# Optimization experiments

Measured on AMD Instinct MI355X. Metric: run time of the kernel, lower is better.

## Reference

```python
import jax, jax.numpy as jnp
import numpy as np

N_HEADS = 12
D_MODEL = 768
D_HEAD = 64
N_CTX = 2048
ROTARY_DIM = 64
ROTARY_BASE = 10000.0
IGNORE = -100000.0


def _sin_cos_rotary(rotary_dim, n_ctx, base):
    # rotary_adjacent_pairs = False -> freq tiled as (2 d)
    pos = jnp.arange(n_ctx, dtype=jnp.float32)
    dim = jnp.arange(rotary_dim // 2, dtype=jnp.float32)
    freq = base ** (dim / (rotary_dim / 2))
    freq = jnp.concatenate([freq, freq])  # '(2 d)'
    angles = pos[:, None] / freq[None, :]  # [n_ctx, rotary_dim]
    return jnp.sin(angles), jnp.cos(angles)


def _apply_rotary(x, sin, cos):
    # x: [B, S, H, d_head]
    S = x.shape[1]
    x_rot = x[..., :ROTARY_DIM]
    x_pass = x[..., ROTARY_DIM:]
    n = ROTARY_DIM // 2
    # rotate: first half <- -second half, second half <- first half
    x_flip = jnp.concatenate([-x_rot[..., n:], x_rot[..., :n]], axis=-1)
    c = cos[None, :S, None, :]
    s = sin[None, :S, None, :]
    return jnp.concatenate([x_rot * c + x_flip * s, x_pass], axis=-1)


def setup_inputs() -> dict:
    key = jax.random.key(0)
    ks = jax.random.split(key, 10)
    B, S = 2, 2048
    x_shape = (B, S, N_HEADS, D_MODEL)
    inp = {
        "normalized_resid_pre_q": jax.random.normal(ks[0], x_shape, jnp.float32),
        "normalized_resid_pre_k": jax.random.normal(ks[1], x_shape, jnp.float32),
        "normalized_resid_pre_v": jax.random.normal(ks[2], x_shape, jnp.float32),
        "W_Q": jax.random.normal(ks[3], (N_HEADS, D_MODEL, D_HEAD), jnp.float32) * 0.02,
        "b_Q": jnp.zeros((N_HEADS, D_HEAD), jnp.float32),
        "W_K": jax.random.normal(ks[4], (N_HEADS, D_MODEL, D_HEAD), jnp.float32) * 0.02,
        "b_K": jnp.zeros((N_HEADS, D_HEAD), jnp.float32),
        "W_V": jax.random.normal(ks[5], (N_HEADS, D_MODEL, D_HEAD), jnp.float32) * 0.02,
        "b_V": jnp.zeros((N_HEADS, D_HEAD), jnp.float32),
        "W_O": jax.random.normal(ks[6], (N_HEADS, D_HEAD, D_MODEL), jnp.float32) * 0.02,
        "b_O": jnp.zeros((D_MODEL,), jnp.float32),
    }
    return inp


def reference(normalized_resid_pre_q, normalized_resid_pre_k, normalized_resid_pre_v,
              W_Q, b_Q, W_K, b_K, W_V, b_V, W_O, b_O):
    sin, cos = _sin_cos_rotary(ROTARY_DIM, N_CTX, ROTARY_BASE)
    # per-head QKV projections: [B,S,H,M] x [H,M,D] -> [B,S,H,D]
    q = jnp.einsum('bshm,hmd->bshd', normalized_resid_pre_q, W_Q) + b_Q
    k = jnp.einsum('bshm,hmd->bshd', normalized_resid_pre_k, W_K) + b_K
    q = _apply_rotary(q, sin, cos)
    k = _apply_rotary(k, sin, cos)
    scores = jnp.einsum('bqhd,bkhd->bhqk', q, k) / jnp.sqrt(jnp.float32(D_HEAD))
    S = scores.shape[-1]
    causal = jnp.triu(jnp.ones((S, S), dtype=bool), k=1)
    scores = jnp.where(causal, jnp.float32(IGNORE), scores)
    pattern = jax.nn.softmax(scores, axis=-1)
    v = jnp.einsum('bkhm,hmd->bkhd', normalized_resid_pre_v, W_V) + b_V
    z = jnp.einsum('bhqk,bkhd->bqhd', pattern, v)
    # output keeps the head axis: [B,S,H,d_model]; b_O is divided by n_heads
    attn_out = jnp.einsum('bqhd,hdm->bqhm', z, W_O) + b_O / N_HEADS
    return attn_out
```

## Files before the change

kernel.cpp:

```cpp
#include <hip/hip_runtime.h>
#include <hip/hip_bf16.h>

typedef __bf16 bf16x8 __attribute__((ext_vector_type(8)));
typedef float f32x4 __attribute__((ext_vector_type(4)));
typedef unsigned short ushort8 __attribute__((ext_vector_type(8)));

static_assert(sizeof(bf16x8) == 16, "bf16x8 must be 16B");

#define NH 12
#define SEQ 2048
#define DM 768
#define DH 64
#define NB 2

static __device__ __forceinline__ unsigned short f2bf(float f) {
    __hip_bfloat16 h = __float2bfloat16(f);
    return __builtin_bit_cast(unsigned short, h);
}
static __device__ __forceinline__ bf16x8 ld_bf8(const unsigned short* p) {
    ushort8 u = *(const ushort8*)p;
    return __builtin_bit_cast(bf16x8, u);
}

__global__ __launch_bounds__(256) void kprep(
    const float* __restrict__ WQ, const float* __restrict__ WK,
    const float* __restrict__ WV, const float* __restrict__ WO,
    unsigned short* __restrict__ Wt, unsigned short* __restrict__ Wot)
{
    __shared__ __align__(16) unsigned short T[64 * 72];
    int bid = blockIdx.x;
    int tensor = bid / 144;
    int rem = bid % 144;
    int h = rem / 12, tile = rem % 12;
    const float* src; unsigned short* dst; int R, C, r0, c0;
    if (tensor < 3) {
        src = (tensor == 0 ? WQ : tensor == 1 ? WK : WV) + (size_t)h * DM * DH;
        dst = Wt + ((size_t)tensor * NH + h) * DH * DM;
        R = DM; C = DH; r0 = tile * 64; c0 = 0;
    } else {
        src = WO + (size_t)h * DH * DM;
        dst = Wot + (size_t)h * DM * DH;
        R = DH; C = DM; r0 = 0; c0 = tile * 64;
    }
    int t = threadIdx.x;
    int rr = t >> 2, cc0 = (t & 3) * 16;
    const float* sp = src + (size_t)(r0 + rr) * C + c0 + cc0;
#pragma unroll
    for (int i = 0; i < 4; i++) {
        float4 v = *(const float4*)(sp + 4 * i);
        T[(cc0 + 4 * i + 0) * 72 + rr] = f2bf(v.x);
        T[(cc0 + 4 * i + 1) * 72 + rr] = f2bf(v.y);
        T[(cc0 + 4 * i + 2) * 72 + rr] = f2bf(v.z);
        T[(cc0 + 4 * i + 3) * 72 + rr] = f2bf(v.w);
    }
    __syncthreads();
    int cc = t >> 2, ch = t & 3;
    ushort8 o0 = *(const ushort8*)&T[cc * 72 + ch * 16];
    ushort8 o1 = *(const ushort8*)&T[cc * 72 + ch * 16 + 8];
    unsigned short* dp = dst + (size_t)(c0 + cc) * R + r0 + ch * 16;
    *(ushort8*)dp = o0;
    *(ushort8*)(dp + 8) = o1;
}

__global__ __launch_bounds__(256) void kproj(
    const float* __restrict__ Xq, const float* __restrict__ Xk,
    const float* __restrict__ Xv, const unsigned short* __restrict__ Wt,
    const float* __restrict__ bQ, const float* __restrict__ bK,
    const float* __restrict__ bV,
    unsigned short* __restrict__ Qw, unsigned short* __restrict__ Kw,
    unsigned short* __restrict__ Vtw)
{
    __shared__ __align__(16) unsigned short sm[64 * 72];
    int bid = blockIdx.x;
    int p  = bid / 768;
    int b  = (bid / 384) & 1;
    int h  = (bid / 32) % 12;
    int st = bid & 31;
    const float* X = p == 0 ? Xq : (p == 1 ? Xk : Xv);
    int t = threadIdx.x;
    int w = t >> 6, lane = t & 63, l = lane & 15, quad = lane >> 4;

    const float* xrow = X + (((size_t)(b * SEQ + st * 64 + 16 * w + l)) * NH + h) * DM + quad * 8;
    const unsigned short* wbase = Wt + ((size_t)(p * NH + h)) * DH * DM;

    f32x4 acc[4] = {};
    for (int k0 = 0; k0 < DM; k0 += 32) {
        float4 f0 = *(const float4*)(xrow + k0);
        float4 f1 = *(const float4*)(xrow + k0 + 4);
        ushort8 u;
        u[0] = f2bf(f0.x); u[1] = f2bf(f0.y); u[2] = f2bf(f0.z); u[3] = f2bf(f0.w);
        u[4] = f2bf(f1.x); u[5] = f2bf(f1.y); u[6] = f2bf(f1.z); u[7] = f2bf(f1.w);
        bf16x8 a = __builtin_bit_cast(bf16x8, u);
#pragma unroll
        for (int nt = 0; nt < 4; nt++) {
            bf16x8 bf = ld_bf8(wbase + ((size_t)(16 * nt + l)) * DM + k0 + quad * 8);
            acc[nt] = __builtin_amdgcn_mfma_f32_16x16x32_bf16(a, bf, acc[nt], 0, 0, 0);
        }
    }

    const float* bias = p == 0 ? bQ : (p == 1 ? bK : bV);
#pragma unroll
    for (int nt = 0; nt < 4; nt++) {
        float bv = bias[h * DH + 16 * nt + l];
#pragma unroll
        for (int r = 0; r < 4; r++) acc[nt][r] += bv;
    }

    if (p < 2) {
        const float L2B = 13.287712379549449f;
        float inv1 = exp2f(-((float)l)        * (L2B / 32.0f));
        float inv2 = exp2f(-((float)(l + 16)) * (L2B / 32.0f));
#pragma unroll
        for (int r = 0; r < 4; r++) {
            float pos = (float)(st * 64 + 16 * w + quad * 4 + r);
            float s1, c1, s2, c2;
            sincosf(pos * inv1, &s1, &c1);
            sincosf(pos * inv2, &s2, &c2);
            float a0 = acc[0][r], a1 = acc[1][r], a2 = acc[2][r], a3 = acc[3][r];
            acc[0][r] = a0 * c1 - a2 * s1;
            acc[1][r] = a1 * c2 - a3 * s2;
            acc[2][r] = a2 * c1 + a0 * s1;
            acc[3][r] = a3 * c2 + a1 * s2;
        }
        unsigned short* dst = (p == 0 ? Qw : Kw) + (((size_t)(b * NH + h)) * SEQ + st * 64) * DH;
#pragma unroll
        for (int nt = 0; nt < 4; nt++)
#pragma unroll
            for (int r = 0; r < 4; r++)
                dst[(16 * w + quad * 4 + r) * DH + 16 * nt + l] = f2bf(acc[nt][r]);
    } else {
#pragma unroll
        for (int nt = 0; nt < 4; nt++)
#pragma unroll
            for (int r = 0; r < 4; r++)
                sm[(16 * nt + l) * 72 + 16 * w + quad * 4 + r] = f2bf(acc[nt][r]);
        __syncthreads();
        int d = t >> 2, c = t & 3;
        ushort8 v0 = *(const ushort8*)&sm[d * 72 + c * 16];
        ushort8 v1 = *(const ushort8*)&sm[d * 72 + c * 16 + 8];
        unsigned short* dp = Vtw + (((size_t)(b * NH + h)) * DH + d) * SEQ + st * 64 + c * 16;
        *(ushort8*)dp = v0;
        *(ushort8*)(dp + 8) = v1;
    }
}

__global__ __launch_bounds__(256) void kattn(
    const unsigned short* __restrict__ Qw, const unsigned short* __restrict__ Kw,
    const unsigned short* __restrict__ Vtw, unsigned short* __restrict__ Zw)
{
    __shared__ __align__(16) unsigned short sK[64 * 72];
    __shared__ __align__(16) unsigned short sV[64 * 72];
    __shared__ __align__(16) unsigned short sP[64 * 72];
    int bid = blockIdx.x;
    int b = bid / 384;
    int h = (bid / 32) % 12;
    int qt = 31 - (bid & 31);
    int t = threadIdx.x;
    int w = t >> 6, lane = t & 63, l = lane & 15, quad = lane >> 4;
    int q0 = qt * 64;

    const unsigned short* qbase = Qw + (((size_t)(b * NH + h)) * SEQ + q0 + 16 * w + l) * DH;
    bf16x8 qf0 = ld_bf8(qbase + quad * 8);
    bf16x8 qf1 = ld_bf8(qbase + 32 + quad * 8);

    const unsigned short* kb = Kw + ((size_t)(b * NH + h)) * SEQ * DH;
    const unsigned short* vb = Vtw + ((size_t)(b * NH + h)) * DH * SEQ;

    int srow = t >> 2, sc = (t & 3) * 16;

    float m_i[4], l_i[4];
    f32x4 zacc[4] = {};
#pragma unroll
    for (int r = 0; r < 4; r++) { m_i[r] = -1e30f; l_i[r] = 0.0f; }

    for (int kt = 0; kt <= qt; kt++) {
        __syncthreads();
        {
            const unsigned short* ks = kb + (size_t)(kt * 64 + srow) * DH + sc;
            ushort8 a0 = *(const ushort8*)ks;
            ushort8 a1 = *(const ushort8*)(ks + 8);
            *(ushort8*)&sK[srow * 72 + sc] = a0;
            *(ushort8*)&sK[srow * 72 + sc + 8] = a1;
            const unsigned short* vs = vb + (size_t)srow * SEQ + kt * 64 + sc;
            ushort8 b0 = *(const ushort8*)vs;
            ushort8 b1 = *(const ushort8*)(vs + 8);
            *(ushort8*)&sV[srow * 72 + sc] = b0;
            *(ushort8*)&sV[srow * 72 + sc + 8] = b1;
        }
        __syncthreads();

        f32x4 sacc[4] = {};
#pragma unroll
        for (int nt = 0; nt < 4; nt++) {
            bf16x8 k0f = __builtin_bit_cast(bf16x8, *(const ushort8*)&sK[(16 * nt + l) * 72 + quad * 8]);
            sacc[nt] = __builtin_amdgcn_mfma_f32_16x16x32_bf16(qf0, k0f, sacc[nt], 0, 0, 0);
            bf16x8 k1f = __builtin_bit_cast(bf16x8, *(const ushort8*)&sK[(16 * nt + l) * 72 + 32 + quad * 8]);
            sacc[nt] = __builtin_amdgcn_mfma_f32_16x16x32_bf16(qf1, k1f, sacc[nt], 0, 0, 0);
        }
        bool diag = (kt == qt);
#pragma unroll
        for (int nt = 0; nt < 4; nt++)
#pragma unroll
            for (int r = 0; r < 4; r++) {
                float s = sacc[nt][r] * 0.125f;
                if (diag && (16 * nt + l) > (16 * w + quad * 4 + r)) s = -1e30f;
                sacc[nt][r] = s;
            }
        float newm[4], alpha[4];
#pragma unroll
        for (int r = 0; r < 4; r++) {
            float rm = fmaxf(fmaxf(sacc[0][r], sacc[1][r]), fmaxf(sacc[2][r], sacc[3][r]));
            rm = fmaxf(rm, __shfl_xor(rm, 1));
            rm = fmaxf(rm, __shfl_xor(rm, 2));
            rm = fmaxf(rm, __shfl_xor(rm, 4));
            rm = fmaxf(rm, __shfl_xor(rm, 8));
            float nm = fmaxf(m_i[r], rm);
            alpha[r] = __expf(m_i[r] - nm);
            m_i[r] = nm;
            newm[r] = nm;
        }
#pragma unroll
        for (int r = 0; r < 4; r++) {
            float rs = 0.0f;
#pragma unroll
            for (int nt = 0; nt < 4; nt++) {
                float pv = __expf(sacc[nt][r] - newm[r]);
                sacc[nt][r] = pv;
                rs += pv;
            }
            rs += __shfl_xor(rs, 1);
            rs += __shfl_xor(rs, 2);
            rs += __shfl_xor(rs, 4);
            rs += __shfl_xor(rs, 8);
            l_i[r] = l_i[r] * alpha[r] + rs;
            zacc[0][r] *= alpha[r]; zacc[1][r] *= alpha[r];
            zacc[2][r] *= alpha[r]; zacc[3][r] *= alpha[r];
        }
#pragma unroll
        for (int nt = 0; nt < 4; nt++)
#pragma unroll
            for (int r = 0; r < 4; r++)
                sP[(w * 16 + quad * 4 + r) * 72 + 16 * nt + l] = f2bf(sacc[nt][r]);
        __asm__ volatile("s_waitcnt lgkmcnt(0)" ::: "memory");
        bf16x8 pa0 = __builtin_bit_cast(bf16x8, *(const ushort8*)&sP[(w * 16 + l) * 72 + quad * 8]);
        bf16x8 pa1 = __builtin_bit_cast(bf16x8, *(const ushort8*)&sP[(w * 16 + l) * 72 + 32 + quad * 8]);
#pragma unroll
        for (int nt = 0; nt < 4; nt++) {
            bf16x8 v0f = __builtin_bit_cast(bf16x8, *(const ushort8*)&sV[(16 * nt + l) * 72 + quad * 8]);
            zacc[nt] = __builtin_amdgcn_mfma_f32_16x16x32_bf16(pa0, v0f, zacc[nt], 0, 0, 0);
            bf16x8 v1f = __builtin_bit_cast(bf16x8, *(const ushort8*)&sV[(16 * nt + l) * 72 + 32 + quad * 8]);
            zacc[nt] = __builtin_amdgcn_mfma_f32_16x16x32_bf16(pa1, v1f, zacc[nt], 0, 0, 0);
        }
    }
    unsigned short* zb = Zw + (((size_t)(b * NH + h)) * SEQ + q0) * DH;
#pragma unroll
    for (int r = 0; r < 4; r++) {
        float inv = 1.0f / l_i[r];
#pragma unroll
        for (int nt = 0; nt < 4; nt++)
            zb[(16 * w + quad * 4 + r) * DH + 16 * nt + l] = f2bf(zacc[nt][r] * inv);
    }
}

__global__ __launch_bounds__(256) void kout(
    const unsigned short* __restrict__ Zw, const unsigned short* __restrict__ Wot,
    const float* __restrict__ bO, float* __restrict__ out)
{
    int bid = blockIdx.x;
    int b = bid / 384;
    int h = (bid / 32) % 12;
    int st = bid & 31;
    int t = threadIdx.x;
    int w = t >> 6, lane = t & 63, l = lane & 15, quad = lane >> 4;

    const unsigned short* zbase = Zw + (((size_t)(b * NH + h)) * SEQ + st * 64 + 16 * w + l) * DH;
    bf16x8 za0 = ld_bf8(zbase + quad * 8);
    bf16x8 za1 = ld_bf8(zbase + 32 + quad * 8);
    const unsigned short* wbase = Wot + (size_t)h * DM * DH;
    float* obase = out + ((size_t)(b * SEQ + st * 64) * NH + h) * DM;

    for (int chunk = 0; chunk < 6; chunk++) {
        f32x4 acc[8] = {};
#pragma unroll
        for (int nt = 0; nt < 8; nt++) {
            int m = chunk * 128 + 16 * nt + l;
            bf16x8 w0 = ld_bf8(wbase + (size_t)m * DH + quad * 8);
            acc[nt] = __builtin_amdgcn_mfma_f32_16x16x32_bf16(za0, w0, acc[nt], 0, 0, 0);
            bf16x8 w1 = ld_bf8(wbase + (size_t)m * DH + 32 + quad * 8);
            acc[nt] = __builtin_amdgcn_mfma_f32_16x16x32_bf16(za1, w1, acc[nt], 0, 0, 0);
        }
#pragma unroll
        for (int nt = 0; nt < 8; nt++) {
            int m = chunk * 128 + 16 * nt + l;
            float bo = bO[m] * (1.0f / 12.0f);
#pragma unroll
            for (int r = 0; r < 4; r++) {
                int srow = 16 * w + quad * 4 + r;
                obase[(size_t)srow * NH * DM + m] = acc[nt][r] + bo;
            }
        }
    }
}

extern "C" void kernel_launch(void* const* d_in, const int* in_sizes, int n_in,
                              void* d_out, int out_size, void* d_ws, size_t ws_size,
                              hipStream_t stream) {
    const float* Xq = (const float*)d_in[0];
    const float* Xk = (const float*)d_in[1];
    const float* Xv = (const float*)d_in[2];
    const float* WQ = (const float*)d_in[3];
    const float* bQ = (const float*)d_in[4];
    const float* WK = (const float*)d_in[5];
    const float* bK = (const float*)d_in[6];
    const float* WV = (const float*)d_in[7];
    const float* bV = (const float*)d_in[8];
    const float* WO = (const float*)d_in[9];
    const float* bO = (const float*)d_in[10];
    float* out = (float*)d_out;

    char* ws = (char*)d_ws;
    size_t o = 0;
    const size_t qkv_bytes = (size_t)NB * NH * SEQ * DH * 2;
    unsigned short* Qw  = (unsigned short*)(ws + o); o += qkv_bytes;
    unsigned short* Kw  = (unsigned short*)(ws + o); o += qkv_bytes;
    unsigned short* Vtw = (unsigned short*)(ws + o); o += qkv_bytes;
    unsigned short* Zw  = (unsigned short*)(ws + o); o += qkv_bytes;
    unsigned short* Wt  = (unsigned short*)(ws + o); o += (size_t)3 * NH * DH * DM * 2;
    unsigned short* Wot = (unsigned short*)(ws + o); o += (size_t)NH * DM * DH * 2;

    kprep<<<dim3(576), dim3(256), 0, stream>>>(WQ, WK, WV, WO, Wt, Wot);
    kproj<<<dim3(2304), dim3(256), 0, stream>>>(Xq, Xk, Xv, Wt, bQ, bK, bV, Qw, Kw, Vtw);
    kattn<<<dim3(768), dim3(256), 0, stream>>>(Qw, Kw, Vtw, Zw);
    kout<<<dim3(768), dim3(256), 0, stream>>>(Zw, Wot, bO, out);
}
```

Baseline: 651.3 us.

## Batch projection loads, stage Q/K stores via LDS, prefetch K/V tiles, split output kernel

The projection kernel now loads four K-steps of X at once and gathers the weight fragments before each group of MFMAs, which gives more memory-level parallelism. Q/K results are staged through LDS so they can be written to global memory as 16-byte vectors instead of scattered 2-byte stores. The attention kernel prefetches the next K/V tile into registers while the current tile is being computed. The output kernel is split six ways across the model dimension to get more blocks, at the cost of reloading the Z fragments in each block.

New measurement: 627.5 us. -3.7%, faster.

```diff
diff --git a/kernel.cpp b/kernel.cpp
--- a/kernel.cpp
+++ b/kernel.cpp
@@ -19,6 +19,12 @@
 }
 static __device__ __forceinline__ bf16x8 ld_bf8(const unsigned short* p) {
     ushort8 u = *(const ushort8*)p;
+    return __builtin_bit_cast(bf16x8, u);
+}
+static __device__ __forceinline__ bf16x8 pack8(float4 f0, float4 f1) {
+    ushort8 u;
+    u[0] = f2bf(f0.x); u[1] = f2bf(f0.y); u[2] = f2bf(f0.z); u[3] = f2bf(f0.w);
+    u[4] = f2bf(f1.x); u[5] = f2bf(f1.y); u[6] = f2bf(f1.z); u[7] = f2bf(f1.w);
     return __builtin_bit_cast(bf16x8, u);
 }
 
@@ -81,20 +87,26 @@
     int w = t >> 6, lane = t & 63, l = lane & 15, quad = lane >> 4;
 
     const float* xrow = X + (((size_t)(b * SEQ + st * 64 + 16 * w + l)) * NH + h) * DM + quad * 8;
-    const unsigned short* wbase = Wt + ((size_t)(p * NH + h)) * DH * DM;
+    const unsigned short* wbase = Wt + ((size_t)(p * NH + h)) * DH * DM + (size_t)l * DM + quad * 8;
 
     f32x4 acc[4] = {};
-    for (int k0 = 0; k0 < DM; k0 += 32) {
-        float4 f0 = *(const float4*)(xrow + k0);
-        float4 f1 = *(const float4*)(xrow + k0 + 4);
-        ushort8 u;
-        u[0] = f2bf(f0.x); u[1] = f2bf(f0.y); u[2] = f2bf(f0.z); u[3] = f2bf(f0.w);
-        u[4] = f2bf(f1.x); u[5] = f2bf(f1.y); u[6] = f2bf(f1.z); u[7] = f2bf(f1.w);
-        bf16x8 a = __builtin_bit_cast(bf16x8, u);
-#pragma unroll
-        for (int nt = 0; nt < 4; nt++) {
-            bf16x8 bf = ld_bf8(wbase + ((size_t)(16 * nt + l)) * DM + k0 + quad * 8);
-            acc[nt] = __builtin_amdgcn_mfma_f32_16x16x32_bf16(a, bf, acc[nt], 0, 0, 0);
+    for (int k0 = 0; k0 < DM; k0 += 128) {
+        float4 xa[8];
+#pragma unroll
+        for (int u = 0; u < 4; u++) {
+            xa[2 * u]     = *(const float4*)(xrow + k0 + 32 * u);
+            xa[2 * u + 1] = *(const float4*)(xrow + k0 + 32 * u + 4);
+        }
+#pragma unroll
+        for (int u = 0; u < 4; u++) {
+            bf16x8 wf[4];
+#pragma unroll
+            for (int nt = 0; nt < 4; nt++)
+                wf[nt] = ld_bf8(wbase + (size_t)nt * 16 * DM + k0 + 32 * u);
+            bf16x8 a = pack8(xa[2 * u], xa[2 * u + 1]);
+#pragma unroll
+            for (int nt = 0; nt < 4; nt++)
+                acc[nt] = __builtin_amdgcn_mfma_f32_16x16x32_bf16(a, wf[nt], acc[nt], 0, 0, 0);
         }
     }
 
@@ -122,12 +134,19 @@
             acc[2][r] = a2 * c1 + a0 * s1;
             acc[3][r] = a3 * c2 + a1 * s2;
         }
-        unsigned short* dst = (p == 0 ? Qw : Kw) + (((size_t)(b * NH + h)) * SEQ + st * 64) * DH;
 #pragma unroll
         for (int nt = 0; nt < 4; nt++)
 #pragma unroll
             for (int r = 0; r < 4; r++)
-                dst[(16 * w + quad * 4 + r) * DH + 16 * nt + l] = f2bf(acc[nt][r]);
+                sm[(16 * w + quad * 4 + r) * 72 + 16 * nt + l] = f2bf(acc[nt][r]);
+        __asm__ volatile("s_waitcnt lgkmcnt(0)" ::: "memory");
+        int local = t & 63;
+        int row = 16 * w + (local >> 2), c = local & 3;
+        ushort8 q0 = *(const ushort8*)&sm[row * 72 + c * 16];
+        ushort8 q1 = *(const ushort8*)&sm[row * 72 + c * 16 + 8];
+        unsigned short* dst = (p == 0 ? Qw : Kw) + (((size_t)(b * NH + h)) * SEQ + st * 64 + row) * DH + c * 16;
+        *(ushort8*)dst = q0;
+        *(ushort8*)(dst + 8) = q1;
     } else {
 #pragma unroll
         for (int nt = 0; nt < 4; nt++)
@@ -173,21 +192,30 @@
 #pragma unroll
     for (int r = 0; r < 4; r++) { m_i[r] = -1e30f; l_i[r] = 0.0f; }
 
+    ushort8 pk0, pk1, pv0, pv1;
+    {
+        const unsigned short* ks = kb + (size_t)srow * DH + sc;
+        pk0 = *(const ushort8*)ks;
+        pk1 = *(const ushort8*)(ks + 8);
+        const unsigned short* vs = vb + (size_t)srow * SEQ + sc;
+        pv0 = *(const ushort8*)vs;
+        pv1 = *(const ushort8*)(vs + 8);
+    }
+
     for (int kt = 0; kt <= qt; kt++) {
+        *(ushort8*)&sK[srow * 72 + sc] = pk0;
+        *(ushort8*)&sK[srow * 72 + sc + 8] = pk1;
+        *(ushort8*)&sV[srow * 72 + sc] = pv0;
+        *(ushort8*)&sV[srow * 72 + sc + 8] = pv1;
         __syncthreads();
-        {
-            const unsigned short* ks = kb + (size_t)(kt * 64 + srow) * DH + sc;
-            ushort8 a0 = *(const ushort8*)ks;
-            ushort8 a1 = *(const ushort8*)(ks + 8);
-            *(ushort8*)&sK[srow * 72 + sc] = a0;
-            *(ushort8*)&sK[srow * 72 + sc + 8] = a1;
-            const unsigned short* vs = vb + (size_t)srow * SEQ + kt * 64 + sc;
-            ushort8 b0 = *(const ushort8*)vs;
-            ushort8 b1 = *(const ushort8*)(vs + 8);
-            *(ushort8*)&sV[srow * 72 + sc] = b0;
-            *(ushort8*)&sV[srow * 72 + sc + 8] = b1;
-        }
-        __syncthreads();
+        if (kt < qt) {
+            const unsigned short* ks = kb + (size_t)((kt + 1) * 64 + srow) * DH + sc;
+            pk0 = *(const ushort8*)ks;
+            pk1 = *(const ushort8*)(ks + 8);
+            const unsigned short* vs = vb + (size_t)srow * SEQ + (kt + 1) * 64 + sc;
+            pv0 = *(const ushort8*)vs;
+            pv1 = *(const ushort8*)(vs + 8);
+        }
 
         f32x4 sacc[4] = {};
 #pragma unroll
@@ -251,6 +279,7 @@
             bf16x8 v1f = __builtin_bit_cast(bf16x8, *(const ushort8*)&sV[(16 * nt + l) * 72 + 32 + quad * 8]);
             zacc[nt] = __builtin_amdgcn_mfma_f32_16x16x32_bf16(pa1, v1f, zacc[nt], 0, 0, 0);
         }
+        __syncthreads();
     }
     unsigned short* zb = Zw + (((size_t)(b * NH + h)) * SEQ + q0) * DH;
 #pragma unroll
@@ -267,37 +296,36 @@
     const float* __restrict__ bO, float* __restrict__ out)
 {
     int bid = blockIdx.x;
-    int b = bid / 384;
-    int h = (bid / 32) % 12;
-    int st = bid & 31;
+    int chunk = bid % 6;
+    int bh = bid / 6;
+    int b = bh / 384;
+    int h = (bh / 32) % 12;
+    int st = bh & 31;
     int t = threadIdx.x;
     int w = t >> 6, lane = t & 63, l = lane & 15, quad = lane >> 4;
 
     const unsigned short* zbase = Zw + (((size_t)(b * NH + h)) * SEQ + st * 64 + 16 * w + l) * DH;
     bf16x8 za0 = ld_bf8(zbase + quad * 8);
     bf16x8 za1 = ld_bf8(zbase + 32 + quad * 8);
-    const unsigned short* wbase = Wot + (size_t)h * DM * DH;
-    float* obase = out + ((size_t)(b * SEQ + st * 64) * NH + h) * DM;
-
-    for (int chunk = 0; chunk < 6; chunk++) {
-        f32x4 acc[8] = {};
-#pragma unroll
-        for (int nt = 0; nt < 8; nt++) {
-            int m = chunk * 128 + 16 * nt + l;
-            bf16x8 w0 = ld_bf8(wbase + (size_t)m * DH + quad * 8);
-            acc[nt] = __builtin_amdgcn_mfma_f32_16x16x32_bf16(za0, w0, acc[nt], 0, 0, 0);
-            bf16x8 w1 = ld_bf8(wbase + (size_t)m * DH + 32 + quad * 8);
-            acc[nt] = __builtin_amdgcn_mfma_f32_16x16x32_bf16(za1, w1, acc[nt], 0, 0, 0);
-        }
-#pragma unroll
-        for (int nt = 0; nt < 8; nt++) {
-            int m = chunk * 128 + 16 * nt + l;
-            float bo = bO[m] * (1.0f / 12.0f);
-#pragma unroll
-            for (int r = 0; r < 4; r++) {
-                int srow = 16 * w + quad * 4 + r;
-                obase[(size_t)srow * NH * DM + m] = acc[nt][r] + bo;
-            }
+    const unsigned short* wbase = Wot + (size_t)h * DM * DH + (size_t)(chunk * 128 + l) * DH + quad * 8;
+    float* obase = out + ((size_t)(b * SEQ + st * 64) * NH + h) * DM + chunk * 128;
+
+    f32x4 acc[8] = {};
+#pragma unroll
+    for (int nt = 0; nt < 8; nt++) {
+        bf16x8 w0 = ld_bf8(wbase + (size_t)nt * 16 * DH);
+        acc[nt] = __builtin_amdgcn_mfma_f32_16x16x32_bf16(za0, w0, acc[nt], 0, 0, 0);
+        bf16x8 w1 = ld_bf8(wbase + (size_t)nt * 16 * DH + 32);
+        acc[nt] = __builtin_amdgcn_mfma_f32_16x16x32_bf16(za1, w1, acc[nt], 0, 0, 0);
+    }
+#pragma unroll
+    for (int nt = 0; nt < 8; nt++) {
+        int m = 16 * nt + l;
+        float bo = bO[chunk * 128 + m] * (1.0f / 12.0f);
+#pragma unroll
+        for (int r = 0; r < 4; r++) {
+            int srow = 16 * w + quad * 4 + r;
+            obase[(size_t)srow * NH * DM + m] = acc[nt][r] + bo;
         }
     }
 }
@@ -331,5 +359,5 @@
     kprep<<<dim3(576), dim3(256), 0, stream>>>(WQ, WK, WV, WO, Wt, Wot);
     kproj<<<dim3(2304), dim3(256), 0, stream>>>(Xq, Xk, Xv, Wt, bQ, bK, bV, Qw, Kw, Vtw);
     kattn<<<dim3(768), dim3(256), 0, stream>>>(Qw, Kw, Vtw, Zw);
-    kout<<<dim3(768), dim3(256), 0, stream>>>(Zw, Wot, bO, out);
-}
+    kout<<<dim3(4608), dim3(256), 0, stream>>>(Zw, Wot, bO, out);
+}
```
